# Kernel tuning notes

Measured on AMD Instinct MI355X. Metric: run time of the kernel, lower is better.

Reference implementation:

```python
import jax, jax.numpy as jnp
import numpy as np

B, N, F = 256, 32, 256
NUM_PASSING = 2


def _fc_edges(n):
    # all ordered pairs (send -> rec), i != j, matching NRI-style encode matrices
    send, rec = [], []
    for i in range(n):
        for j in range(n):
            if i != j:
                send.append(i)
                rec.append(j)
    return np.array(send, np.int32), np.array(rec, np.int32)


def setup_inputs() -> dict:
    key = jax.random.key(0)
    ks = jax.random.split(key, 16)
    send_np, rec_np = _fc_edges(N)

    def xavier(k, shape):
        fan_in, fan_out = shape
        std = (2.0 / (fan_in + fan_out)) ** 0.5
        return jax.random.normal(k, shape, jnp.float32) * std

    bias = lambda d: jnp.full((d,), 0.1, jnp.float32)
    return {
        "x": jax.random.normal(ks[0], (B, N, F), jnp.float32),
        "rec_idx": jnp.asarray(rec_np),
        "send_idx": jnp.asarray(send_np),
        "w_in1": xavier(ks[1], (F, 256)), "b_in1": bias(256),
        "w_in2": xavier(ks[2], (256, 256)), "b_in2": bias(256),
        "w_e1": xavier(ks[3], (512, 256)), "b_e1": bias(256),
        "w_e2": xavier(ks[4], (256, 256)), "b_e2": bias(256),
        "w_n1": xavier(ks[5], (256, 256)), "b_n1": bias(256),
        "w_n2": xavier(ks[6], (256, 256)), "b_n2": bias(256),
    }


def _mlp(h, wa, ba, wb, bb):
    # Linear -> ReLU -> (Dropout p=0) -> Linear -> ReLU
    return jax.nn.relu(jax.nn.relu(h @ wa + ba) @ wb + bb)


def reference(x, rec_idx, send_idx,
              w_in1, b_in1, w_in2, b_in2,
              w_e1, b_e1, w_e2, b_e2,
              w_n1, b_n1, w_n2, b_n2):
    n_nodes = x.shape[-2]
    # in-degree per node == rec_encode.sum(0)
    deg = jax.ops.segment_sum(jnp.ones_like(rec_idx, x.dtype), rec_idx,
                              num_segments=n_nodes)  # [N]
    h = _mlp(x, w_in1, b_in1, w_in2, b_in2)  # [B, N, 256]
    for _ in range(NUM_PASSING):
        # node2edge: gather (== one-hot matmul), cat [sends, recs]
        edges = jnp.concatenate([h[:, send_idx, :], h[:, rec_idx, :]], axis=-1)  # [B, E, 512]
        e = _mlp(edges, w_e1, b_e1, w_e2, b_e2)  # [B, E, 256]
        # edge2node: scatter-sum by receiver then divide by in-degree (mean)
        e_t = jnp.swapaxes(e, 0, 1)  # [E, B, 256]
        agg = jax.ops.segment_sum(e_t, rec_idx, num_segments=n_nodes)  # [N, B, 256]
        agg = jnp.swapaxes(agg, 0, 1) / deg[None, :, None]  # [B, N, 256]
        h = _mlp(agg, w_n1, b_n1, w_n2, b_n2)
    return h
```

## Files before the change

kernel.cpp:

```cpp
#include <hip/hip_runtime.h>


typedef short bf16x8 __attribute__((ext_vector_type(8)));
typedef float f32x4 __attribute__((ext_vector_type(4)));
typedef unsigned short ushort_t;

__device__ __forceinline__ unsigned short f2bf(float f) {
    unsigned u = __float_as_uint(f);
    u += 0x7fff + ((u >> 16) & 1);
    return (unsigned short)(u >> 16);
}
__device__ __forceinline__ float lo16f(unsigned w) { return __uint_as_float(w << 16); }
__device__ __forceinline__ float hi16f(unsigned w) { return __uint_as_float(w & 0xffff0000u); }
__device__ __forceinline__ unsigned cvt_pk_bf16(float lo, float hi) {
    unsigned r;
    asm volatile("v_cvt_pk_bf16_f32 %0, %1, %2" : "=v"(r) : "v"(lo), "v"(hi));
    return r;
}
__device__ __forceinline__ void gload16(const void* g, void* l) {
    __builtin_amdgcn_global_load_lds(
        (const __attribute__((address_space(1))) void*)g,
        (__attribute__((address_space(3))) void*)l, 16, 0, 0);
}

__global__ __launch_bounds__(256) void prep_weights(
    const float* __restrict__ w_in1, const float* __restrict__ w_in2,
    const float* __restrict__ w_e1,  const float* __restrict__ w_e2,
    const float* __restrict__ w_n1,  const float* __restrict__ w_n2,
    ushort_t* __restrict__ dst)
{
    __shared__ ushort_t tile[32][264];
    const int wid = blockIdx.x >> 3;
    const int kb  = blockIdx.x & 7;
    const float* src;
    switch (wid) {
        case 0: src = w_in1; break;
        case 1: src = w_in2; break;
        case 2: src = w_e1; break;
        case 3: src = w_e1 + 65536; break;
        case 4: src = w_e2; break;
        case 5: src = w_n1; break;
        default: src = w_n2; break;
    }
    const int t = threadIdx.x;
#pragma unroll
    for (int k0 = 0; k0 < 32; k0++)
        tile[k0][t] = f2bf(src[(size_t)(kb * 32 + k0) * 256 + t]);
    __syncthreads();
    ushort_t* base = dst + wid * 65536 + kb * 8192 + t * 32;
    const int sw = (t >> 1) & 3;
#pragma unroll
    for (int kc = 0; kc < 4; kc++) {
        union { uint4 q; ushort_t u[8]; } w;
#pragma unroll
        for (int ko = 0; ko < 8; ko++) w.u[ko] = tile[kc * 8 + ko][t];
        *(uint4*)&base[(kc ^ sw) * 8] = w.q;
    }
}

__global__ __launch_bounds__(256) void conv_x(
    const float* __restrict__ x, ushort_t* __restrict__ xb, int n8)
{
    int i = blockIdx.x * 256 + threadIdx.x;
    if (i >= n8) return;
    const float4* p = (const float4*)x + (size_t)i * 2;
    float4 a = p[0], b = p[1];
    ushort4 o0 = make_ushort4(f2bf(a.x), f2bf(a.y), f2bf(a.z), f2bf(a.w));
    ushort4 o1 = make_ushort4(f2bf(b.x), f2bf(b.y), f2bf(b.z), f2bf(b.w));
    ((ushort4*)xb)[(size_t)i * 2]     = o0;
    ((ushort4*)xb)[(size_t)i * 2 + 1] = o1;
}


__device__ __forceinline__ void layer_to_lds(
    const ushort_t* __restrict__ wimg, const float* __restrict__ bias,
    const ushort_t* __restrict__ As, ushort_t* __restrict__ Ad,
    const int w, const int lr, const int lg)
{
    int boffs[4]; float4 b4[4];
#pragma unroll
    for (int fn = 0; fn < 4; fn++) {
        const int n = w * 64 + fn * 16 + lr;
        boffs[fn] = n * 32 + ((lg ^ ((n >> 1) & 3)) * 8);
        b4[fn] = *(const float4*)&bias[w * 64 + fn * 16 + lg * 4];
    }
    bf16x8 bc[4];
#pragma unroll
    for (int fn = 0; fn < 4; fn++) bc[fn] = *(const bf16x8*)&wimg[boffs[fn]];
    f32x4 acc[4][2] = {};
#pragma unroll
    for (int kb = 0; kb < 8; kb++) {
        bf16x8 bn[4];
        if (kb < 7)
#pragma unroll
            for (int fn = 0; fn < 4; fn++)
                bn[fn] = *(const bf16x8*)&wimg[(kb + 1) * 8192 + boffs[fn]];
        bf16x8 af[2];
#pragma unroll
        for (int fm = 0; fm < 2; fm++) {
            const int r = fm * 16 + lr;
            af[fm] = *(const bf16x8*)&As[r * 256 + (((kb * 4 + lg) ^ (r & 7)) * 8)];
        }
#pragma unroll
        for (int fn = 0; fn < 4; fn++)
#pragma unroll
            for (int fm = 0; fm < 2; fm++)
                acc[fn][fm] = __builtin_amdgcn_mfma_f32_16x16x32_bf16(
                    bc[fn], af[fm], acc[fn][fm], 0, 0, 0);
        if (kb < 7)
#pragma unroll
            for (int fn = 0; fn < 4; fn++) bc[fn] = bn[fn];
    }
#pragma unroll
    for (int fn = 0; fn < 4; fn++) {
        const int k0 = w * 64 + fn * 16 + lg * 4;
        const int kc = k0 >> 3, kj = k0 & 7;
#pragma unroll
        for (int fm = 0; fm < 2; fm++) {
            const int m = fm * 16 + lr;
            float v0 = fmaxf(acc[fn][fm][0] + b4[fn].x, 0.f);
            float v1 = fmaxf(acc[fn][fm][1] + b4[fn].y, 0.f);
            float v2 = fmaxf(acc[fn][fm][2] + b4[fn].z, 0.f);
            float v3 = fmaxf(acc[fn][fm][3] + b4[fn].w, 0.f);
            uint2 q = { cvt_pk_bf16(v0, v1), cvt_pk_bf16(v2, v3) };
            *(uint2*)&Ad[m * 256 + ((kc ^ (m & 7)) * 8) + kj] = q;
        }
    }
}

__device__ __forceinline__ void layer_e1(
    const ushort_t* __restrict__ wE, const float* __restrict__ bE,
    const ushort_t* __restrict__ As, ushort_t* __restrict__ UVb,
    const int m0, const int w, const int lr, const int lg)
{
    const ushort_t* wimg = (w < 2) ? wE : (wE + 65536);
    const int nb = (w & 1) * 128;
    int boffs[8]; float4 b4[8];
#pragma unroll
    for (int fn = 0; fn < 8; fn++) {
        const int n = nb + fn * 16 + lr;
        boffs[fn] = n * 32 + ((lg ^ ((n >> 1) & 3)) * 8);
        if (w < 2) b4[fn] = *(const float4*)&bE[nb + fn * 16 + lg * 4];
        else       b4[fn] = make_float4(0.f, 0.f, 0.f, 0.f);
    }
    bf16x8 bc[8];
#pragma unroll
    for (int fn = 0; fn < 8; fn++) bc[fn] = *(const bf16x8*)&wimg[boffs[fn]];
    f32x4 acc[8][2] = {};
#pragma unroll
    for (int kb = 0; kb < 8; kb++) {
        bf16x8 bn[8];
        if (kb < 7)
#pragma unroll
            for (int fn = 0; fn < 8; fn++)
                bn[fn] = *(const bf16x8*)&wimg[(kb + 1) * 8192 + boffs[fn]];
        bf16x8 af[2];
#pragma unroll
        for (int fm = 0; fm < 2; fm++) {
            const int r = fm * 16 + lr;
            af[fm] = *(const bf16x8*)&As[r * 256 + (((kb * 4 + lg) ^ (r & 7)) * 8)];
        }
#pragma unroll
        for (int fn = 0; fn < 8; fn++)
#pragma unroll
            for (int fm = 0; fm < 2; fm++)
                acc[fn][fm] = __builtin_amdgcn_mfma_f32_16x16x32_bf16(
                    bc[fn], af[fm], acc[fn][fm], 0, 0, 0);
        if (kb < 7)
#pragma unroll
            for (int fn = 0; fn < 8; fn++) bc[fn] = bn[fn];
    }
#pragma unroll
    for (int fn = 0; fn < 8; fn++) {
        const int nglob = w * 128 + fn * 16 + lg * 4;
#pragma unroll
        for (int fm = 0; fm < 2; fm++) {
            const int node = m0 + fm * 16 + lr;
            float v0 = acc[fn][fm][0] + b4[fn].x;
            float v1 = acc[fn][fm][1] + b4[fn].y;
            float v2 = acc[fn][fm][2] + b4[fn].z;
            float v3 = acc[fn][fm][3] + b4[fn].w;
            uint2 q = { cvt_pk_bf16(v0, v1), cvt_pk_bf16(v2, v3) };
            *(uint2*)&UVb[(size_t)node * 512 + nglob] = q;
        }
    }
}

__device__ __forceinline__ void layer_fin(
    const ushort_t* __restrict__ wimg, const float* __restrict__ bias,
    const ushort_t* __restrict__ As, float* __restrict__ out,
    const int m0, const int w, const int lr, const int lg)
{
    int boffs[4]; float4 b4[4];
#pragma unroll
    for (int fn = 0; fn < 4; fn++) {
        const int n = w * 64 + fn * 16 + lr;
        boffs[fn] = n * 32 + ((lg ^ ((n >> 1) & 3)) * 8);
        b4[fn] = *(const float4*)&bias[w * 64 + fn * 16 + lg * 4];
    }
    bf16x8 bc[4];
#pragma unroll
    for (int fn = 0; fn < 4; fn++) bc[fn] = *(const bf16x8*)&wimg[boffs[fn]];
    f32x4 acc[4][2] = {};
#pragma unroll
    for (int kb = 0; kb < 8; kb++) {
        bf16x8 bn[4];
        if (kb < 7)
#pragma unroll
            for (int fn = 0; fn < 4; fn++)
                bn[fn] = *(const bf16x8*)&wimg[(kb + 1) * 8192 + boffs[fn]];
        bf16x8 af[2];
#pragma unroll
        for (int fm = 0; fm < 2; fm++) {
            const int r = fm * 16 + lr;
            af[fm] = *(const bf16x8*)&As[r * 256 + (((kb * 4 + lg) ^ (r & 7)) * 8)];
        }
#pragma unroll
        for (int fn = 0; fn < 4; fn++)
#pragma unroll
            for (int fm = 0; fm < 2; fm++)
                acc[fn][fm] = __builtin_amdgcn_mfma_f32_16x16x32_bf16(
                    bc[fn], af[fm], acc[fn][fm], 0, 0, 0);
        if (kb < 7)
#pragma unroll
            for (int fn = 0; fn < 4; fn++) bc[fn] = bn[fn];
    }
#pragma unroll
    for (int fn = 0; fn < 4; fn++) {
        const int col = w * 64 + fn * 16 + lg * 4;
#pragma unroll
        for (int fm = 0; fm < 2; fm++) {
            const int row = m0 + fm * 16 + lr;
            float4 o;
            o.x = fmaxf(acc[fn][fm][0] + b4[fn].x, 0.f);
            o.y = fmaxf(acc[fn][fm][1] + b4[fn].y, 0.f);
            o.z = fmaxf(acc[fn][fm][2] + b4[fn].z, 0.f);
            o.w = fmaxf(acc[fn][fm][3] + b4[fn].w, 0.f);
            *(float4*)&out[(size_t)row * 256 + col] = o;
        }
    }
}

template <int THREE>
__global__ __launch_bounds__(256, 2) void mlp_chain(
    const ushort_t* __restrict__ in,
    const ushort_t* __restrict__ wA, const float* __restrict__ bA,
    const ushort_t* __restrict__ wB, const float* __restrict__ bB,
    const ushort_t* __restrict__ wE, const float* __restrict__ bE,
    void* __restrict__ out)
{
    __shared__ ushort_t A0[32 * 256];
    __shared__ ushort_t A1[32 * 256];
    const int m0 = blockIdx.x * 32;
    const int t = threadIdx.x;
    const int lane = t & 63, w = t >> 6;
    const int lr = lane & 15, lg = lane >> 4;

#pragma unroll
    for (int i = 0; i < 4; i++) {
        const int r = i * 8 + (t >> 5);
        const int p = t & 31;
        gload16(in + (size_t)(m0 + r) * 256 + ((p ^ (r & 7)) * 8), &A0[i * 2048 + t * 8]);
    }
    __syncthreads();

    layer_to_lds(wA, bA, A0, A1, w, lr, lg);
    __syncthreads();
    if constexpr (THREE) {
        layer_to_lds(wB, bB, A1, A0, w, lr, lg);
        __syncthreads();
        layer_e1(wE, bE, A0, (ushort_t*)out, m0, w, lr, lg);
    } else {
        layer_fin(wB, bB, A1, (float*)out, m0, w, lr, lg);
    }
}

__global__ __launch_bounds__(256, 2) void edge_fused(
    const ushort_t* __restrict__ UVb,
    const ushort_t* __restrict__ WBsw,
    const float* __restrict__ b2,
    ushort_t* __restrict__ agg)
{
    __shared__ ushort_t As[2][128 * 64];

    const int logical = (blockIdx.x & 7) * 256 + (blockIdx.x >> 3);
    const int bb = logical >> 3;
    const int g0 = (logical & 7) * 4;
    const int t = threadIdx.x;
    const int lane = t & 63;
    const int w = t >> 6;
    const int lr = lane & 15, lg = lane >> 4;

    const int brow = t >> 1;
    const int kh = t & 1;
    const int jr = brow >> 5;
    const int s = brow & 31;
    const int j = g0 + jr;
    const int si = (s == 31) ? j : (s + (s >= j ? 1 : 0));
    const ushort_t* up = UVb + (size_t)(bb * 32 + si) * 512 + kh * 32;
    const ushort_t* vp = UVb + (size_t)(bb * 32 + j) * 512 + 256 + kh * 32;
    const int rs7 = brow & 7;
    int aw[4];
#pragma unroll
    for (int i = 0; i < 4; i++)
        aw[i] = brow * 64 + (((kh * 4 + i) ^ rs7) * 8);

    const int acof0 = ((lg ^ (lr & 7)) * 8) + lr * 64;
    const int bbase = (w * 64 + lr) * 32 + ((lg ^ ((lr >> 1) & 3)) * 8);

    auto build = [&](int buf, const uint4* u, const uint4* v) {
#pragma unroll
        for (int i = 0; i < 4; i++) {
            uint4 q;
            q.x = cvt_pk_bf16(fmaxf(lo16f(u[i].x) + lo16f(v[i].x), 0.f),
                              fmaxf(hi16f(u[i].x) + hi16f(v[i].x), 0.f));
            q.y = cvt_pk_bf16(fmaxf(lo16f(u[i].y) + lo16f(v[i].y), 0.f),
                              fmaxf(hi16f(u[i].y) + hi16f(v[i].y), 0.f));
            q.z = cvt_pk_bf16(fmaxf(lo16f(u[i].z) + lo16f(v[i].z), 0.f),
                              fmaxf(hi16f(u[i].z) + hi16f(v[i].z), 0.f));
            q.w = cvt_pk_bf16(fmaxf(lo16f(u[i].w) + lo16f(v[i].w), 0.f),
                              fmaxf(hi16f(u[i].w) + hi16f(v[i].w), 0.f));
            *(uint4*)&As[buf][aw[i]] = q;
        }
    };

    {
        uint4 u[4], v[4];
#pragma unroll
        for (int i = 0; i < 4; i++) {
            u[i] = *(const uint4*)(up + i * 8);
            v[i] = *(const uint4*)(vp + i * 8);
        }
        build(0, u, v);
    }
    bf16x8 bc[2][4];
#pragma unroll
    for (int ks = 0; ks < 2; ks++)
#pragma unroll
        for (int fn = 0; fn < 4; fn++)
            bc[ks][fn] = *(const bf16x8*)&WBsw[ks * 8192 + bbase + fn * 512];

    f32x4 acc[8][4] = {};

#pragma unroll
    for (int kb = 0; kb < 4; kb++) {
        __syncthreads();
        uint4 u[4], v[4];
        if (kb < 3) {
            const ushort_t* upn = up + (kb + 1) * 64;
            const ushort_t* vpn = vp + (kb + 1) * 64;
#pragma unroll
            for (int i = 0; i < 4; i++) {
                u[i] = *(const uint4*)(upn + i * 8);
                v[i] = *(const uint4*)(vpn + i * 8);
            }
        }
        __builtin_amdgcn_s_setprio(1);
#pragma unroll
        for (int ks = 0; ks < 2; ks++) {
            bf16x8 af[8];
#pragma unroll
            for (int m = 0; m < 8; m++)
                af[m] = *(const bf16x8*)&As[kb & 1][m * 1024 + (acof0 ^ (ks * 32))];
#pragma unroll
            for (int fn = 0; fn < 4; fn++)
#pragma unroll
                for (int m = 0; m < 8; m++)
                    acc[m][fn] = __builtin_amdgcn_mfma_f32_16x16x32_bf16(
                        af[m], bc[ks][fn], acc[m][fn], 0, 0, 0);
        }
        __builtin_amdgcn_s_setprio(0);
        if (kb < 3) {
#pragma unroll
            for (int ks = 0; ks < 2; ks++)
#pragma unroll
                for (int fn = 0; fn < 4; fn++)
                    bc[ks][fn] = *(const bf16x8*)&WBsw[((kb + 1) * 2 + ks) * 8192
                                                       + bbase + fn * 512];
            build((kb + 1) & 1, u, v);
        }
    }

#pragma unroll
    for (int fn = 0; fn < 4; fn++) {
        const int col = w * 64 + fn * 16 + lr;
        const float bvf = b2[col];
#pragma unroll
        for (int recv = 0; recv < 4; recv++) {
            float sum = 0.f;
#pragma unroll
            for (int q = 0; q < 2; q++) {
                const int fm = recv * 2 + q;
#pragma unroll
                for (int r = 0; r < 4; r++) {
                    float v = fmaxf(acc[fm][fn][r] + bvf, 0.f);
                    if (!(q == 1 && lg == 3 && r == 3)) sum += v;
                }
            }
            sum += __shfl_xor(sum, 16);
            sum += __shfl_xor(sum, 32);
            if (lane < 16)
                agg[(size_t)(bb * 32 + g0 + recv) * 256 + col] = f2bf(sum * (1.0f / 31.0f));
        }
    }
}

extern "C" void kernel_launch(void* const* d_in, const int* in_sizes, int n_in,
                              void* d_out, int out_size, void* d_ws, size_t ws_size,
                              hipStream_t stream)
{
    const float* x     = (const float*)d_in[0];
    const float* w_in1 = (const float*)d_in[3];
    const float* b_in1 = (const float*)d_in[4];
    const float* w_in2 = (const float*)d_in[5];
    const float* b_in2 = (const float*)d_in[6];
    const float* w_e1  = (const float*)d_in[7];
    const float* b_e1  = (const float*)d_in[8];
    const float* w_e2  = (const float*)d_in[9];
    const float* b_e2  = (const float*)d_in[10];
    const float* w_n1  = (const float*)d_in[11];
    const float* b_n1  = (const float*)d_in[12];
    const float* w_n2  = (const float*)d_in[13];
    const float* b_n2  = (const float*)d_in[14];

    char* ws = (char*)d_ws;
    size_t off = 0;
    auto alloc = [&](size_t n) { char* p = ws + off; off += (n + 255) & ~(size_t)255; return p; };

    ushort_t* wt  = (ushort_t*)alloc(7 * 65536 * sizeof(ushort_t));
    ushort_t* xb  = (ushort_t*)alloc(8192 * 256 * 2);
    ushort_t* UVb = (ushort_t*)alloc(8192 * 512 * 2);
    ushort_t* ag  = (ushort_t*)alloc(8192 * 256 * 2);
    (void)ws_size; (void)in_sizes; (void)n_in; (void)out_size;

    prep_weights<<<56, 256, 0, stream>>>(w_in1, w_in2, w_e1, w_e2, w_n1, w_n2, wt);
    conv_x<<<1024, 256, 0, stream>>>(x, xb, 262144);

    mlp_chain<1><<<256, 256, 0, stream>>>(xb,
        wt + 0 * 65536, b_in1, wt + 1 * 65536, b_in2, wt + 2 * 65536, b_e1, UVb);
    edge_fused<<<2048, 256, 0, stream>>>(UVb, wt + 4 * 65536, b_e2, ag);
    mlp_chain<1><<<256, 256, 0, stream>>>(ag,
        wt + 5 * 65536, b_n1, wt + 6 * 65536, b_n2, wt + 2 * 65536, b_e1, UVb);
    edge_fused<<<2048, 256, 0, stream>>>(UVb, wt + 4 * 65536, b_e2, ag);
    mlp_chain<0><<<256, 256, 0, stream>>>(ag,
        wt + 5 * 65536, b_n1, wt + 6 * 65536, b_n2, nullptr, nullptr, d_out);
}
```

Measured before the change: 134.2 us.

## Merge prep kernels, deepen weight prefetch, split e1 layer, soften edge barrier

Merges the weight-conversion and x-conversion kernels into one launch to remove a kernel boundary. The global weight-fragment prefetch in the MLP layers becomes a three-slot ring that loads two k-blocks ahead, which hides more load latency at the cost of more registers. layer_e1 is split into two 64-column halves to lower register pressure. In edge_fused, __syncthreads is replaced by a barrier that waits only on LDS/scalar counters, so outstanding global loads stay in flight across it.

```diff
diff --git a/kernel.cpp b/kernel.cpp
--- a/kernel.cpp
+++ b/kernel.cpp
@@ -22,14 +22,31 @@
         (const __attribute__((address_space(1))) void*)g,
         (__attribute__((address_space(3))) void*)l, 16, 0, 0);
 }
-
-__global__ __launch_bounds__(256) void prep_weights(
+__device__ __forceinline__ void soft_barrier() {
+    asm volatile("s_waitcnt lgkmcnt(0)" ::: "memory");
+    __builtin_amdgcn_sched_barrier(0);
+    __builtin_amdgcn_s_barrier();
+}
+
+__global__ __launch_bounds__(256) void prep_all(
     const float* __restrict__ w_in1, const float* __restrict__ w_in2,
     const float* __restrict__ w_e1,  const float* __restrict__ w_e2,
     const float* __restrict__ w_n1,  const float* __restrict__ w_n2,
-    ushort_t* __restrict__ dst)
+    ushort_t* __restrict__ dst,
+    const float* __restrict__ x, ushort_t* __restrict__ xb)
 {
     __shared__ ushort_t tile[32][264];
+    const int t = threadIdx.x;
+    if (blockIdx.x >= 56) {
+        const int i = (blockIdx.x - 56) * 256 + t;
+        const float4* p = (const float4*)x + (size_t)i * 2;
+        float4 a = p[0], b = p[1];
+        ushort4 o0 = make_ushort4(f2bf(a.x), f2bf(a.y), f2bf(a.z), f2bf(a.w));
+        ushort4 o1 = make_ushort4(f2bf(b.x), f2bf(b.y), f2bf(b.z), f2bf(b.w));
+        ((ushort4*)xb)[(size_t)i * 2]     = o0;
+        ((ushort4*)xb)[(size_t)i * 2 + 1] = o1;
+        return;
+    }
     const int wid = blockIdx.x >> 3;
     const int kb  = blockIdx.x & 7;
     const float* src;
@@ -42,7 +59,6 @@
         case 5: src = w_n1; break;
         default: src = w_n2; break;
     }
-    const int t = threadIdx.x;
 #pragma unroll
     for (int k0 = 0; k0 < 32; k0++)
         tile[k0][t] = f2bf(src[(size_t)(kb * 32 + k0) * 256 + t]);
@@ -58,19 +74,6 @@
     }
 }
 
-__global__ __launch_bounds__(256) void conv_x(
-    const float* __restrict__ x, ushort_t* __restrict__ xb, int n8)
-{
-    int i = blockIdx.x * 256 + threadIdx.x;
-    if (i >= n8) return;
-    const float4* p = (const float4*)x + (size_t)i * 2;
-    float4 a = p[0], b = p[1];
-    ushort4 o0 = make_ushort4(f2bf(a.x), f2bf(a.y), f2bf(a.z), f2bf(a.w));
-    ushort4 o1 = make_ushort4(f2bf(b.x), f2bf(b.y), f2bf(b.z), f2bf(b.w));
-    ((ushort4*)xb)[(size_t)i * 2]     = o0;
-    ((ushort4*)xb)[(size_t)i * 2 + 1] = o1;
-}
-
 
 __device__ __forceinline__ void layer_to_lds(
     const ushort_t* __restrict__ wimg, const float* __restrict__ bias,
@@ -84,17 +87,18 @@
         boffs[fn] = n * 32 + ((lg ^ ((n >> 1) & 3)) * 8);
         b4[fn] = *(const float4*)&bias[w * 64 + fn * 16 + lg * 4];
     }
-    bf16x8 bc[4];
-#pragma unroll
-    for (int fn = 0; fn < 4; fn++) bc[fn] = *(const bf16x8*)&wimg[boffs[fn]];
+    bf16x8 bq[3][4];
+#pragma unroll
+    for (int fn = 0; fn < 4; fn++) bq[0][fn] = *(const bf16x8*)&wimg[boffs[fn]];
+#pragma unroll
+    for (int fn = 0; fn < 4; fn++) bq[1][fn] = *(const bf16x8*)&wimg[8192 + boffs[fn]];
     f32x4 acc[4][2] = {};
 #pragma unroll
     for (int kb = 0; kb < 8; kb++) {
-        bf16x8 bn[4];
-        if (kb < 7)
+        if (kb < 6)
 #pragma unroll
             for (int fn = 0; fn < 4; fn++)
-                bn[fn] = *(const bf16x8*)&wimg[(kb + 1) * 8192 + boffs[fn]];
+                bq[(kb + 2) % 3][fn] = *(const bf16x8*)&wimg[(kb + 2) * 8192 + boffs[fn]];
         bf16x8 af[2];
 #pragma unroll
         for (int fm = 0; fm < 2; fm++) {
@@ -106,10 +110,7 @@
 #pragma unroll
             for (int fm = 0; fm < 2; fm++)
                 acc[fn][fm] = __builtin_amdgcn_mfma_f32_16x16x32_bf16(
-                    bc[fn], af[fm], acc[fn][fm], 0, 0, 0);
-        if (kb < 7)
-#pragma unroll
-            for (int fn = 0; fn < 4; fn++) bc[fn] = bn[fn];
+                    bq[kb % 3][fn], af[fm], acc[fn][fm], 0, 0, 0);
     }
 #pragma unroll
     for (int fn = 0; fn < 4; fn++) {
@@ -134,54 +135,55 @@
     const int m0, const int w, const int lr, const int lg)
 {
     const ushort_t* wimg = (w < 2) ? wE : (wE + 65536);
-    const int nb = (w & 1) * 128;
-    int boffs[8]; float4 b4[8];
-#pragma unroll
-    for (int fn = 0; fn < 8; fn++) {
-        const int n = nb + fn * 16 + lr;
-        boffs[fn] = n * 32 + ((lg ^ ((n >> 1) & 3)) * 8);
-        if (w < 2) b4[fn] = *(const float4*)&bE[nb + fn * 16 + lg * 4];
-        else       b4[fn] = make_float4(0.f, 0.f, 0.f, 0.f);
-    }
-    bf16x8 bc[8];
-#pragma unroll
-    for (int fn = 0; fn < 8; fn++) bc[fn] = *(const bf16x8*)&wimg[boffs[fn]];
-    f32x4 acc[8][2] = {};
-#pragma unroll
-    for (int kb = 0; kb < 8; kb++) {
-        bf16x8 bn[8];
-        if (kb < 7)
-#pragma unroll
-            for (int fn = 0; fn < 8; fn++)
-                bn[fn] = *(const bf16x8*)&wimg[(kb + 1) * 8192 + boffs[fn]];
-        bf16x8 af[2];
-#pragma unroll
-        for (int fm = 0; fm < 2; fm++) {
-            const int r = fm * 16 + lr;
-            af[fm] = *(const bf16x8*)&As[r * 256 + (((kb * 4 + lg) ^ (r & 7)) * 8)];
-        }
-#pragma unroll
-        for (int fn = 0; fn < 8; fn++)
-#pragma unroll
-            for (int fm = 0; fm < 2; fm++)
-                acc[fn][fm] = __builtin_amdgcn_mfma_f32_16x16x32_bf16(
-                    bc[fn], af[fm], acc[fn][fm], 0, 0, 0);
-        if (kb < 7)
-#pragma unroll
-            for (int fn = 0; fn < 8; fn++) bc[fn] = bn[fn];
-    }
-#pragma unroll
-    for (int fn = 0; fn < 8; fn++) {
-        const int nglob = w * 128 + fn * 16 + lg * 4;
-#pragma unroll
-        for (int fm = 0; fm < 2; fm++) {
-            const int node = m0 + fm * 16 + lr;
-            float v0 = acc[fn][fm][0] + b4[fn].x;
-            float v1 = acc[fn][fm][1] + b4[fn].y;
-            float v2 = acc[fn][fm][2] + b4[fn].z;
-            float v3 = acc[fn][fm][3] + b4[fn].w;
-            uint2 q = { cvt_pk_bf16(v0, v1), cvt_pk_bf16(v2, v3) };
-            *(uint2*)&UVb[(size_t)node * 512 + nglob] = q;
+#pragma unroll
+    for (int g = 0; g < 2; g++) {
+        const int nb = (w & 1) * 128 + g * 64;
+        int boffs[4]; float4 b4[4];
+#pragma unroll
+        for (int fn = 0; fn < 4; fn++) {
+            const int n = nb + fn * 16 + lr;
+            boffs[fn] = n * 32 + ((lg ^ ((n >> 1) & 3)) * 8);
+            if (w < 2) b4[fn] = *(const float4*)&bE[nb + fn * 16 + lg * 4];
+            else       b4[fn] = make_float4(0.f, 0.f, 0.f, 0.f);
+        }
+        bf16x8 bq[3][4];
+#pragma unroll
+        for (int fn = 0; fn < 4; fn++) bq[0][fn] = *(const bf16x8*)&wimg[boffs[fn]];
+#pragma unroll
+        for (int fn = 0; fn < 4; fn++) bq[1][fn] = *(const bf16x8*)&wimg[8192 + boffs[fn]];
+        f32x4 acc[4][2] = {};
+#pragma unroll
+        for (int kb = 0; kb < 8; kb++) {
+            if (kb < 6)
+#pragma unroll
+                for (int fn = 0; fn < 4; fn++)
+                    bq[(kb + 2) % 3][fn] = *(const bf16x8*)&wimg[(kb + 2) * 8192 + boffs[fn]];
+            bf16x8 af[2];
+#pragma unroll
+            for (int fm = 0; fm < 2; fm++) {
+                const int r = fm * 16 + lr;
+                af[fm] = *(const bf16x8*)&As[r * 256 + (((kb * 4 + lg) ^ (r & 7)) * 8)];
+            }
+#pragma unroll
+            for (int fn = 0; fn < 4; fn++)
+#pragma unroll
+                for (int fm = 0; fm < 2; fm++)
+                    acc[fn][fm] = __builtin_amdgcn_mfma_f32_16x16x32_bf16(
+                        bq[kb % 3][fn], af[fm], acc[fn][fm], 0, 0, 0);
+        }
+#pragma unroll
+        for (int fn = 0; fn < 4; fn++) {
+            const int nglob = w * 128 + g * 64 + fn * 16 + lg * 4;
+#pragma unroll
+            for (int fm = 0; fm < 2; fm++) {
+                const int node = m0 + fm * 16 + lr;
+                float v0 = acc[fn][fm][0] + b4[fn].x;
+                float v1 = acc[fn][fm][1] + b4[fn].y;
+                float v2 = acc[fn][fm][2] + b4[fn].z;
+                float v3 = acc[fn][fm][3] + b4[fn].w;
+                uint2 q = { cvt_pk_bf16(v0, v1), cvt_pk_bf16(v2, v3) };
+                *(uint2*)&UVb[(size_t)node * 512 + nglob] = q;
+            }
         }
     }
 }
@@ -198,17 +200,18 @@
         boffs[fn] = n * 32 + ((lg ^ ((n >> 1) & 3)) * 8);
         b4[fn] = *(const float4*)&bias[w * 64 + fn * 16 + lg * 4];
     }
-    bf16x8 bc[4];
-#pragma unroll
-    for (int fn = 0; fn < 4; fn++) bc[fn] = *(const bf16x8*)&wimg[boffs[fn]];
+    bf16x8 bq[3][4];
+#pragma unroll
+    for (int fn = 0; fn < 4; fn++) bq[0][fn] = *(const bf16x8*)&wimg[boffs[fn]];
+#pragma unroll
+    for (int fn = 0; fn < 4; fn++) bq[1][fn] = *(const bf16x8*)&wimg[8192 + boffs[fn]];
     f32x4 acc[4][2] = {};
 #pragma unroll
     for (int kb = 0; kb < 8; kb++) {
-        bf16x8 bn[4];
-        if (kb < 7)
+        if (kb < 6)
 #pragma unroll
             for (int fn = 0; fn < 4; fn++)
-                bn[fn] = *(const bf16x8*)&wimg[(kb + 1) * 8192 + boffs[fn]];
+                bq[(kb + 2) % 3][fn] = *(const bf16x8*)&wimg[(kb + 2) * 8192 + boffs[fn]];
         bf16x8 af[2];
 #pragma unroll
         for (int fm = 0; fm < 2; fm++) {
@@ -220,10 +223,7 @@
 #pragma unroll
             for (int fm = 0; fm < 2; fm++)
                 acc[fn][fm] = __builtin_amdgcn_mfma_f32_16x16x32_bf16(
-                    bc[fn], af[fm], acc[fn][fm], 0, 0, 0);
-        if (kb < 7)
-#pragma unroll
-            for (int fn = 0; fn < 4; fn++) bc[fn] = bn[fn];
+                    bq[kb % 3][fn], af[fm], acc[fn][fm], 0, 0, 0);
     }
 #pragma unroll
     for (int fn = 0; fn < 4; fn++) {
@@ -344,7 +344,8 @@
 
 #pragma unroll
     for (int kb = 0; kb < 4; kb++) {
-        __syncthreads();
+        const int cur = kb & 1;
+        soft_barrier();
         uint4 u[4], v[4];
         if (kb < 3) {
             const ushort_t* upn = up + (kb + 1) * 64;
@@ -361,7 +362,7 @@
             bf16x8 af[8];
 #pragma unroll
             for (int m = 0; m < 8; m++)
-                af[m] = *(const bf16x8*)&As[kb & 1][m * 1024 + (acof0 ^ (ks * 32))];
+                af[m] = *(const bf16x8*)&As[cur][m * 1024 + (acof0 ^ (ks * 32))];
 #pragma unroll
             for (int fn = 0; fn < 4; fn++)
 #pragma unroll
@@ -377,7 +378,7 @@
                 for (int fn = 0; fn < 4; fn++)
                     bc[ks][fn] = *(const bf16x8*)&WBsw[((kb + 1) * 2 + ks) * 8192
                                                        + bbase + fn * 512];
-            build((kb + 1) & 1, u, v);
+            build(cur ^ 1, u, v);
         }
     }
 
@@ -433,8 +434,7 @@
     ushort_t* ag  = (ushort_t*)alloc(8192 * 256 * 2);
     (void)ws_size; (void)in_sizes; (void)n_in; (void)out_size;
 
-    prep_weights<<<56, 256, 0, stream>>>(w_in1, w_in2, w_e1, w_e2, w_n1, w_n2, wt);
-    conv_x<<<1024, 256, 0, stream>>>(x, xb, 262144);
+    prep_all<<<1080, 256, 0, stream>>>(w_in1, w_in2, w_e1, w_e2, w_n1, w_n2, wt, x, xb);
 
     mlp_chain<1><<<256, 256, 0, stream>>>(xb,
         wt + 0 * 65536, b_in1, wt + 1 * 65536, b_in2, wt + 2 * 65536, b_e1, UVb);
```

Result: no change. 134.1 us (-0.1%).
